# Kernel optimization log

Hardware: AMD Instinct MI355X
Metric: run time of the kernel (lower is better)

Reference implementation:

```python
import jax, jax.numpy as jnp
import numpy as np

V = 32000      # vocab_size
CTX = 1024     # context_length
D = 768        # n_embd
H = 12         # n_heads
HD = D // H    # head_dim
L = 6          # n_layers
DFF = 4 * D
B, S = 2, 1024
EPS = 1e-5


def _layernorm(x, w, b):
    mu = jnp.mean(x, axis=-1, keepdims=True)
    var = jnp.mean(jnp.square(x - mu), axis=-1, keepdims=True)
    return (x - mu) * jax.lax.rsqrt(var + EPS) * w + b


def setup_inputs() -> dict:
    key = jax.random.key(0)
    ks = iter(jax.random.split(key, 32))
    s = 0.02
    idx = jax.random.randint(next(ks), (B, S), 0, V)
    p = {
        "idx": idx,
        "tok_emb": jax.random.normal(next(ks), (V, D), jnp.float32) * s,
        "pos_emb": jax.random.normal(next(ks), (CTX, D), jnp.float32) * s,
        "ln1_w": jnp.ones((L, D)), "ln1_b": jnp.zeros((L, D)),
        "Wq": jax.random.normal(next(ks), (L, D, D), jnp.float32) * s,
        "bq": jnp.zeros((L, D)),
        "Wk": jax.random.normal(next(ks), (L, D, D), jnp.float32) * s,
        "bk": jnp.zeros((L, D)),
        "Wv": jax.random.normal(next(ks), (L, D, D), jnp.float32) * s,
        "bv": jnp.zeros((L, D)),
        "Wo": jax.random.normal(next(ks), (L, D, D), jnp.float32) * s,
        "bo": jnp.zeros((L, D)),
        "ln2_w": jnp.ones((L, D)), "ln2_b": jnp.zeros((L, D)),
        "W1": jax.random.normal(next(ks), (L, D, DFF), jnp.float32) * s,
        "b1": jnp.zeros((L, DFF)),
        "W2": jax.random.normal(next(ks), (L, DFF, D), jnp.float32) * s,
        "b2": jnp.zeros((L, D)),
        "lnf_w": jnp.ones((D,)), "lnf_b": jnp.zeros((D,)),
        "lm_head_w": jax.random.normal(next(ks), (D, V), jnp.float32) * s,
    }
    return p


def _forward(idx, tok_emb, pos_emb, ln1_w, ln1_b, Wq, bq, Wk, bk, Wv, bv,
             Wo, bo, ln2_w, ln2_b, W1, b1, W2, b2, lnf_w, lnf_b, lm_head_w):
    b, s = idx.shape
    x = tok_emb[idx] + pos_emb[:s]  # [B,S,D]
    mask = jnp.tril(jnp.ones((s, s), dtype=bool))  # causal
    scale = 1.0 / np.sqrt(HD)
    for l in range(L):
        # --- attention ---
        h = _layernorm(x, ln1_w[l], ln1_b[l])
        q = (h @ Wq[l] + bq[l]).reshape(b, s, H, HD).transpose(0, 2, 1, 3)
        k = (h @ Wk[l] + bk[l]).reshape(b, s, H, HD).transpose(0, 2, 1, 3)
        v = (h @ Wv[l] + bv[l]).reshape(b, s, H, HD).transpose(0, 2, 1, 3)
        att = jnp.einsum('bhqd,bhkd->bhqk', q, k) * scale
        att = jnp.where(mask, att, -jnp.inf)
        att = jax.nn.softmax(att, axis=-1)
        y = jnp.einsum('bhqk,bhkd->bhqd', att, v)
        y = y.transpose(0, 2, 1, 3).reshape(b, s, D)
        x = x + y @ Wo[l] + bo[l]
        # --- MLP ---
        h2 = _layernorm(x, ln2_w[l], ln2_b[l])
        x = x + jax.nn.relu(h2 @ W1[l] + b1[l]) @ W2[l] + b2[l]
    logits = _layernorm(x, lnf_w, lnf_b) @ lm_head_w  # [B,S,V]
    return logits


def reference(idx, tok_emb, pos_emb, ln1_w, ln1_b, Wq, bq, Wk, bk, Wv, bv,
              Wo, bo, ln2_w, ln2_b, W1, b1, W2, b2, lnf_w, lnf_b, lm_head_w):
    return _forward(idx, tok_emb, pos_emb, ln1_w, ln1_b, Wq, bq, Wk, bk, Wv,
                    bv, Wo, bo, ln2_w, ln2_b, W1, b1, W2, b2, lnf_w, lnf_b,
                    lm_head_w)
```

## Files before the change

### kernel.cpp

```cpp
#include <hip/hip_runtime.h>
#include <hip/hip_bf16.h>
#include <math.h>

#define D 768
#define NH 12
#define HD 64
#define NL 6
#define DFF 3072
#define BB 2
#define SS 1024
#define NROWS (BB*SS)
#define VOCAB 32000
#define QKVN (3*D)
#define LN_EPS 1e-5f

typedef __attribute__((ext_vector_type(8))) short bf16x8;
typedef __attribute__((ext_vector_type(4))) float f32x4;

typedef __attribute__((address_space(1))) const unsigned char* gas_ptr;
typedef __attribute__((address_space(3))) unsigned char* las_ptr;

__device__ __forceinline__ void load_lds16(const void* g, void* l) {
    __builtin_amdgcn_global_load_lds((gas_ptr)g, (las_ptr)l, 16, 0, 0);
}

__device__ __forceinline__ void storeOut(float* p, float v) { *p = v; }
__device__ __forceinline__ void storeOut(__hip_bfloat16* p, float v) { *p = __float2bfloat16(v); }
__device__ __forceinline__ ushort f2bs(float f) {
    __hip_bfloat16 h = __float2bfloat16(f);
    return *(ushort*)&h;
}

#define WAIT_VMCNT(n) asm volatile("s_waitcnt vmcnt(" #n ")" ::: "memory")

__global__ void embed_kernel(const int* __restrict__ idx, const float* __restrict__ tok,
                             const float* __restrict__ pos, float* __restrict__ x) {
    int row = blockIdx.x;
    int s = row % SS;
    int t = idx[row];
    for (int c = threadIdx.x; c < D; c += blockDim.x)
        x[row*D + c] = tok[(size_t)t*D + c] + pos[s*D + c];
}

template<typename OT>
__global__ __launch_bounds__(256) void layernorm_kernel(const float* __restrict__ x,
                                                        const float* __restrict__ w,
                                                        const float* __restrict__ b,
                                                        OT* __restrict__ out) {
    int row = blockIdx.x;
    __shared__ float l1[4], l2[4];
    int base = row * D;
    float vals[3];
    float s1 = 0.f, s2 = 0.f;
#pragma unroll
    for (int i = 0; i < 3; i++) {
        float v = x[base + threadIdx.x + i*256];
        vals[i] = v; s1 += v; s2 += v*v;
    }
#pragma unroll
    for (int o = 32; o > 0; o >>= 1) {
        s1 += __shfl_down(s1, o, 64);
        s2 += __shfl_down(s2, o, 64);
    }
    if ((threadIdx.x & 63) == 0) { l1[threadIdx.x >> 6] = s1; l2[threadIdx.x >> 6] = s2; }
    __syncthreads();
    float sum   = l1[0] + l1[1] + l1[2] + l1[3];
    float sumsq = l2[0] + l2[1] + l2[2] + l2[3];
    float mu  = sum * (1.f / D);
    float var = sumsq * (1.f / D) - mu * mu;
    float inv = rsqrtf(var + LN_EPS);
#pragma unroll
    for (int i = 0; i < 3; i++) {
        int c = threadIdx.x + i*256;
        storeOut(&out[base + c], (vals[i] - mu) * inv * w[c] + b[c]);
    }
}

__global__ __launch_bounds__(256) void transpose_cvt(const float* __restrict__ src,
                                                     __hip_bfloat16* __restrict__ dst,
                                                     int K, int N,
                                                     size_t srcLayerStride, size_t dstLayerStride,
                                                     int dstRowOff) {
    int l = blockIdx.z;
    src += (size_t)l * srcLayerStride;
    dst += (size_t)l * dstLayerStride + (size_t)dstRowOff * K;
    __shared__ float t[32][33];
    int k0 = blockIdx.x*32, n0 = blockIdx.y*32;
    int tx = threadIdx.x & 31, ty = threadIdx.x >> 5;
    for (int i = ty; i < 32; i += 8) t[i][tx] = src[(size_t)(k0+i)*N + n0+tx];
    __syncthreads();
    for (int i = ty; i < 32; i += 8) dst[(size_t)(n0+i)*K + k0+tx] = __float2bfloat16(t[tx][i]);
}

__global__ __launch_bounds__(256) void qkvo_trans(const float* __restrict__ Wq,
                                                  const float* __restrict__ Wk,
                                                  const float* __restrict__ Wv,
                                                  const float* __restrict__ Wo,
                                                  __hip_bfloat16* __restrict__ qkvT,
                                                  __hip_bfloat16* __restrict__ WoT) {
    int z = blockIdx.z, l = z >> 2, m = z & 3;
    const float* src = (m==0 ? Wq : m==1 ? Wk : m==2 ? Wv : Wo) + (size_t)l*D*D;
    __hip_bfloat16* dst = (m < 3) ? qkvT + (size_t)l*QKVN*D + (size_t)m*D*D
                                  : WoT  + (size_t)l*D*D;
    __shared__ float t[32][33];
    int k0 = blockIdx.x*32, n0 = blockIdx.y*32;
    int tx = threadIdx.x & 31, ty = threadIdx.x >> 5;
    for (int i = ty; i < 32; i += 8) t[i][tx] = src[(size_t)(k0+i)*D + n0+tx];
    __syncthreads();
    for (int i = ty; i < 32; i += 8) dst[(size_t)(n0+i)*D + k0+tx] = __float2bfloat16(t[tx][i]);
}

__global__ void pack_qkv_bias(const float* __restrict__ bq, const float* __restrict__ bk,
                              const float* __restrict__ bv, float* __restrict__ dst) {
    int l = blockIdx.y;
    int i = blockIdx.x*256 + threadIdx.x;
    dst[l*QKVN + i]         = bq[l*D + i];
    dst[l*QKVN + D + i]     = bk[l*D + i];
    dst[l*QKVN + 2*D + i]   = bv[l*D + i];
}

#define GSTAGE(buf, k0) do {                                                     \
    _Pragma("unroll")                                                            \
    for (int i_ = 0; i_ < BM/64; i_++) {                                         \
        int rt_ = wid*(BM/4) + i_*16;                                            \
        load_lds16(A + (size_t)(bm + rt_ + lrow)*K + (k0) + lcol,                \
                   &As[buf][rt_][0]);                                            \
    }                                                                            \
    _Pragma("unroll")                                                            \
    for (int i_ = 0; i_ < BN/64; i_++) {                                         \
        int rt_ = wid*(BN/4) + i_*16;                                            \
        load_lds16(BT + (size_t)(bn + rt_ + lrow)*K + (k0) + lcol,               \
                   &Bs[buf][rt_][0]);                                            \
    } } while (0)

template<int BM, int BN, int CMAJ, typename OT, int RELU, int RESID, int HASB, int VSTORE>
__global__ __launch_bounds__(256) void gemm_mfma(const ushort* __restrict__ A,
                                                 const ushort* __restrict__ BT,
                                                 const float* __restrict__ bias,
                                                 const float* __restrict__ X,
                                                 OT* __restrict__ C,
                                                 ushort* __restrict__ vt,
                                                 int N, int K, int gx, int gy) {
    constexpr int WTM = BM/2, WTN = BN/2;
    constexpr int FRM = BM/32, FRN = BN/32;
    __shared__ ushort As[2][BM][32];
    __shared__ ushort Bs[2][BN][32];

    int id = blockIdx.x;
    int swz = (id & 7) * (gridDim.x >> 3) + (id >> 3);
    int bx, by;
    if (CMAJ) { bx = swz / gy; by = swz - bx * gy; }
    else      { by = swz / gx; bx = swz - by * gx; }
    int bm = by * BM, bn = bx * BN;

    int tid = threadIdx.x;
    int lane = tid & 63, wid = tid >> 6;
    int wr = wid >> 1, wc = wid & 1;
    int lrow = lane >> 2;
    int lcol = (((lane & 3) ^ ((lane >> 3) & 3)) * 8);
    int fr = lane & 15, fc = lane >> 4;
    int rchunk = (fc ^ ((fr >> 1) & 3)) * 8;

    f32x4 acc[FRM][FRN];
#pragma unroll
    for (int i = 0; i < FRM; i++)
#pragma unroll
        for (int j = 0; j < FRN; j++)
#pragma unroll
            for (int r = 0; r < 4; r++) acc[i][j][r] = 0.f;

    GSTAGE(0, 0);
    asm volatile("s_waitcnt vmcnt(0)" ::: "memory");
    __syncthreads();

    int cur = 0;
    for (int t = 0; t < K/32; t++) {
        if (t*32 + 32 < K) GSTAGE(cur^1, t*32 + 32);
        bf16x8 af[FRM], bf[FRN];
#pragma unroll
        for (int mi = 0; mi < FRM; mi++)
            af[mi] = *(const bf16x8*)&As[cur][wr*WTM + mi*16 + fr][rchunk];
#pragma unroll
        for (int ni = 0; ni < FRN; ni++)
            bf[ni] = *(const bf16x8*)&Bs[cur][wc*WTN + ni*16 + fr][rchunk];
        __builtin_amdgcn_s_setprio(1);
#pragma unroll
        for (int mi = 0; mi < FRM; mi++)
#pragma unroll
            for (int ni = 0; ni < FRN; ni++)
                acc[mi][ni] = __builtin_amdgcn_mfma_f32_16x16x32_bf16(af[mi], bf[ni], acc[mi][ni], 0, 0, 0);
        __builtin_amdgcn_s_setprio(0);
        asm volatile("s_waitcnt vmcnt(0)" ::: "memory");
        __syncthreads();
        cur ^= 1;
    }

    if (VSTORE && bn >= 2*D) {
        int hh = (bn - 2*D) / HD;
        int b  = bm >> 10;
        size_t vbase = ((size_t)(b*NH + hh)) * HD;
        int srow0 = (bm & (SS-1)) + wr*WTM + fc*4;
#pragma unroll
        for (int mi = 0; mi < FRM; mi++) {
#pragma unroll
            for (int ni = 0; ni < FRN; ni++) {
                int col = bn + wc*WTN + ni*16 + fr;
                int d   = wc*WTN + ni*16 + fr;
                float bv_ = bias[col];
                ushort4 u;
                u.x = f2bs(acc[mi][ni][0] + bv_);
                u.y = f2bs(acc[mi][ni][1] + bv_);
                u.z = f2bs(acc[mi][ni][2] + bv_);
                u.w = f2bs(acc[mi][ni][3] + bv_);
                *(ushort4*)&vt[(vbase + d)*SS + srow0 + mi*16] = u;
            }
        }
    } else {
#pragma unroll
        for (int mi = 0; mi < FRM; mi++) {
#pragma unroll
            for (int r = 0; r < 4; r++) {
                int row = bm + wr*WTM + mi*16 + fc*4 + r;
#pragma unroll
                for (int ni = 0; ni < FRN; ni++) {
                    int col = bn + wc*WTN + ni*16 + fr;
                    float v = acc[mi][ni][r];
                    if (HASB) v += bias[col];
                    if (RESID) v += X[(size_t)row * N + col];
                    if (RELU) v = fmaxf(v, 0.f);
                    storeOut(&C[(size_t)row * N + col], v);
                }
            }
        }
    }
}

#define RSTAGE(slot, k0) do {                                                    \
    int row_ = tid >> 2;                                                         \
    load_lds16(A  + (size_t)(bm + row_)*K + (k0) + sc_,                          \
               (char*)As + (size_t)(slot)*4096 + (size_t)wid*1024);              \
    load_lds16(BT + (size_t)(bn + row_)*K + (k0) + sc_,                          \
               (char*)Bs + (size_t)(slot)*4096 + (size_t)wid*1024);              \
    } while (0)

template<int RELU>
__global__ __launch_bounds__(256) void gemm_ring64(const ushort* __restrict__ A,
                                                   const ushort* __restrict__ BT,
                                                   const float* __restrict__ bias,
                                                   const float* __restrict__ X,
                                                   float* __restrict__ C,
                                                   int N, int K, int gx) {
    __shared__ ushort As[4][64][32];
    __shared__ ushort Bs[4][64][32];

    int id = blockIdx.x;
    int swz = (id & 7) * (gridDim.x >> 3) + (id >> 3);
    int by = swz / gx, bx = swz - by * gx;
    int bm = by * 64, bn = bx * 64;

    int tid = threadIdx.x;
    int lane = tid & 63, wid = tid >> 6;
    int wr = wid >> 1, wc = wid & 1;
    int sc_ = ((lane & 3) ^ ((lane >> 3) & 3)) * 8;
    int fr = lane & 15, fc = lane >> 4;
    int rchunk = (fc ^ ((fr >> 1) & 3)) * 8;

    f32x4 acc[2][2];
#pragma unroll
    for (int i = 0; i < 2; i++)
#pragma unroll
        for (int j = 0; j < 2; j++)
#pragma unroll
            for (int r = 0; r < 4; r++) acc[i][j][r] = 0.f;

    const int NT = K / 32;
    RSTAGE(0, 0);
    RSTAGE(1, 32);
    RSTAGE(2, 64);

    for (int t = 0; t < NT; t++) {
        if (t < NT-2)      WAIT_VMCNT(4);
        else if (t == NT-2) WAIT_VMCNT(2);
        else               WAIT_VMCNT(0);
        __builtin_amdgcn_s_barrier();
        asm volatile("" ::: "memory");
        if (t + 3 < NT) RSTAGE((t+3) & 3, (t+3)*32);
        int s = t & 3;
        bf16x8 af[2], bf[2];
#pragma unroll
        for (int mi = 0; mi < 2; mi++)
            af[mi] = *(const bf16x8*)&As[s][wr*32 + mi*16 + fr][rchunk];
#pragma unroll
        for (int ni = 0; ni < 2; ni++)
            bf[ni] = *(const bf16x8*)&Bs[s][wc*32 + ni*16 + fr][rchunk];
        __builtin_amdgcn_s_setprio(1);
#pragma unroll
        for (int mi = 0; mi < 2; mi++)
#pragma unroll
            for (int ni = 0; ni < 2; ni++)
                acc[mi][ni] = __builtin_amdgcn_mfma_f32_16x16x32_bf16(af[mi], bf[ni], acc[mi][ni], 0, 0, 0);
        __builtin_amdgcn_s_setprio(0);
    }

#pragma unroll
    for (int mi = 0; mi < 2; mi++) {
#pragma unroll
        for (int r = 0; r < 4; r++) {
            int row = bm + wr*32 + mi*16 + fc*4 + r;
#pragma unroll
            for (int ni = 0; ni < 2; ni++) {
                int col = bn + wc*32 + ni*16 + fr;
                float v = acc[mi][ni][r] + bias[col] + X[(size_t)row * N + col];
                if (RELU) v = fmaxf(v, 0.f);
                C[(size_t)row * N + col] = v;
            }
        }
    }
}

#define LMSA3(slot, k0) do {                                                      \
    _Pragma("unroll")                                                             \
    for (int i_ = 0; i_ < 2; i_++) {                                              \
        int row_ = i_*128 + (tid >> 2);                                           \
        load_lds16(A + (size_t)(bm + row_)*D + (k0) + sc_,                        \
                   (char*)As3 + (size_t)(slot)*16384 + (size_t)(i_*512 + wid*64)*16); \
    } } while (0)
#define LMSB3(slot, k0) do {                                                      \
    _Pragma("unroll")                                                             \
    for (int i_ = 0; i_ < 2; i_++) {                                              \
        int row_ = i_*128 + (tid >> 2);                                           \
        load_lds16(BT + (size_t)(bm_n + row_)*D + (k0) + sc_,                     \
                   (char*)Bs3 + (size_t)(slot)*16384 + (size_t)(i_*512 + wid*64)*16); \
    } } while (0)

__global__ __launch_bounds__(512) void lm256_gemm(const ushort* __restrict__ A,
                                                  const ushort* __restrict__ BT,
                                                  float* __restrict__ C) {
    constexpr int NKT = D / 32;
    __shared__ ushort As3[3][256][32];
    __shared__ ushort Bs3[3][256][32];

    int id = blockIdx.x;
    int swz = (id & 7) * 125 + (id >> 3);
    int by = swz & 7;
    int bx = swz >> 3;
    int bm = by * 256, bm_n = bx * 256;

    int tid = threadIdx.x;
    int lane = tid & 63, wid = tid >> 6;
    int wr = wid >> 2, wc = wid & 3;
    int sc_ = ((tid & 3) ^ ((tid >> 3) & 3)) * 8;
    int fr = lane & 15, fc = lane >> 4;
    int rch = (fc ^ ((fr >> 1) & 3)) * 8;

    f32x4 acc[8][4];
#pragma unroll
    for (int i = 0; i < 8; i++)
#pragma unroll
        for (int j = 0; j < 4; j++)
#pragma unroll
            for (int r = 0; r < 4; r++) acc[i][j][r] = 0.f;

    LMSA3(0, 0);  LMSB3(0, 0);
    LMSA3(1, 32); LMSB3(1, 32);
    WAIT_VMCNT(4);
    __builtin_amdgcn_s_barrier();

    int s = 0;
    for (int j = 0; j < NKT; j++) {
        int s2 = s + 2; if (s2 >= 3) s2 -= 3;
        int kf2 = (j + 2) * 32;
        bf16x8 bfr[4], af[4];
#pragma unroll
        for (int ni = 0; ni < 4; ni++)
            bfr[ni] = *(const bf16x8*)&Bs3[s][wc*64 + ni*16 + fr][rch];
#pragma unroll
        for (int dm = 0; dm < 4; dm++)
            af[dm] = *(const bf16x8*)&As3[s][wr*128 + dm*16 + fr][rch];
        if (j + 2 < NKT) LMSA3(s2, kf2);
        __builtin_amdgcn_s_barrier();
        __builtin_amdgcn_s_setprio(1);
#pragma unroll
        for (int dm = 0; dm < 4; dm++)
#pragma unroll
            for (int ni = 0; ni < 4; ni++)
                acc[dm][ni] = __builtin_amdgcn_mfma_f32_16x16x32_bf16(af[dm], bfr[ni], acc[dm][ni], 0, 0, 0);
        __builtin_amdgcn_s_setprio(0);
        __builtin_amdgcn_s_barrier();
#pragma unroll
        for (int dm = 0; dm < 4; dm++)
            af[dm] = *(const bf16x8*)&As3[s][wr*128 + (4+dm)*16 + fr][rch];
        if (j + 2 < NKT) { LMSB3(s2, kf2); WAIT_VMCNT(2); }
        else             { WAIT_VMCNT(0); }
        __builtin_amdgcn_s_barrier();
        __builtin_amdgcn_s_setprio(1);
#pragma unroll
        for (int dm = 0; dm < 4; dm++)
#pragma unroll
            for (int ni = 0; ni < 4; ni++)
                acc[4+dm][ni] = __builtin_amdgcn_mfma_f32_16x16x32_bf16(af[dm], bfr[ni], acc[4+dm][ni], 0, 0, 0);
        __builtin_amdgcn_s_setprio(0);
        __builtin_amdgcn_s_barrier();
        s = s + 1; if (s >= 3) s = 0;
    }

#pragma unroll
    for (int mi = 0; mi < 8; mi++)
#pragma unroll
        for (int r = 0; r < 4; r++) {
            int row = bm + wr*128 + mi*16 + fc*4 + r;
            float* cp = C + (size_t)row * VOCAB + bm_n + wc*64 + fr;
#pragma unroll
            for (int ni = 0; ni < 4; ni++)
                cp[ni*16] = acc[mi][ni][r];
        }
}

#define KVSTAGE(buf, kv0) do {                                                   \
    _Pragma("unroll")                                                            \
    for (int j_ = 0; j_ < 2; j_++) {                                             \
        int r_ = w*16 + j_*8 + srow8;                                            \
        load_lds16(qkv + (size_t)(b*SS + (kv0) + r_)*QKVN + D + h*HD + schunk*8, \
                   &Ks[buf][w*16 + j_*8][0]);                                    \
        load_lds16(vt + ((size_t)(b*NH + h)*HD + r_)*SS + (kv0) + schunk*8,      \
                   &Vs[buf][w*16 + j_*8][0]);                                    \
    } } while (0)

__global__ __launch_bounds__(256) void attn_mfma(const ushort* __restrict__ qkv,
                                                 const ushort* __restrict__ vt,
                                                 __hip_bfloat16* __restrict__ y) {
    const int bx = blockIdx.x;
    const int qt = 15 - (bx & 15);
    const int h  = (bx >> 4) % NH;
    const int b  = bx / (16*NH);
    const int tid  = threadIdx.x;
    const int lane = tid & 63, w = tid >> 6;
    const int fr = lane & 15, fc = lane >> 4;

    __shared__ ushort Qs[64][64];
    __shared__ ushort Ks[2][64][64];
    __shared__ ushort Vs[2][64][64];
    __shared__ ushort Ps[4][16][72];

    const int q0 = qt * 64;
    const int srow8  = lane >> 3;
    const int schunk = (lane & 7) ^ srow8;

#pragma unroll
    for (int j = 0; j < 2; j++) {
        int r = w*16 + j*8 + srow8;
        load_lds16(qkv + (size_t)(b*SS + q0 + r)*QKVN + h*HD + schunk*8, &Qs[w*16 + j*8][0]);
    }
    KVSTAGE(0, 0);
    asm volatile("s_waitcnt vmcnt(0)" ::: "memory");
    __syncthreads();
    bf16x8 qf[2];
#pragma unroll
    for (int s = 0; s < 2; s++)
        qf[s] = *(const bf16x8*)&Qs[w*16 + fr][((s*4 + fc) ^ (fr & 7))*8];

    f32x4 oacc[4];
#pragma unroll
    for (int ni = 0; ni < 4; ni++)
#pragma unroll
        for (int r = 0; r < 4; r++) oacc[ni][r] = 0.f;
    float m[4] = {-INFINITY, -INFINITY, -INFINITY, -INFINITY};
    float l[4] = {0.f, 0.f, 0.f, 0.f};

    int cur = 0;
    for (int kt = 0; kt <= qt; kt++) {
        if (kt < qt) KVSTAGE(cur^1, (kt+1)*64);
        f32x4 sacc[4];
#pragma unroll
        for (int ni = 0; ni < 4; ni++)
#pragma unroll
            for (int r = 0; r < 4; r++) sacc[ni][r] = 0.f;
#pragma unroll
        for (int ni = 0; ni < 4; ni++)
#pragma unroll
            for (int s = 0; s < 2; s++) {
                bf16x8 kf = *(const bf16x8*)&Ks[cur][ni*16 + fr][((s*4 + fc) ^ (fr & 7))*8];
                sacc[ni] = __builtin_amdgcn_mfma_f32_16x16x32_bf16(qf[s], kf, sacc[ni], 0, 0, 0);
            }
        if (kt == qt) {
#pragma unroll
            for (int ni = 0; ni < 4; ni++)
#pragma unroll
                for (int r = 0; r < 4; r++) {
                    float v = sacc[ni][r] * 0.125f;
                    sacc[ni][r] = (ni*16 + fr > w*16 + fc*4 + r) ? -INFINITY : v;
                }
        } else {
#pragma unroll
            for (int ni = 0; ni < 4; ni++)
#pragma unroll
                for (int r = 0; r < 4; r++) sacc[ni][r] *= 0.125f;
        }
        float p[4][4];
#pragma unroll
        for (int r = 0; r < 4; r++) {
            float mx = fmaxf(fmaxf(sacc[0][r], sacc[1][r]), fmaxf(sacc[2][r], sacc[3][r]));
#pragma unroll
            for (int o = 1; o < 16; o <<= 1) mx = fmaxf(mx, __shfl_xor(mx, o, 64));
            float mn = fmaxf(m[r], mx);
            float fac = __expf(m[r] - mn);
            float rs = 0.f;
#pragma unroll
            for (int ni = 0; ni < 4; ni++) {
                float pv = __expf(sacc[ni][r] - mn);
                p[ni][r] = pv;
                rs += pv;
            }
#pragma unroll
            for (int o = 1; o < 16; o <<= 1) rs += __shfl_xor(rs, o, 64);
            l[r] = l[r] * fac + rs;
            m[r] = mn;
#pragma unroll
            for (int ni = 0; ni < 4; ni++) oacc[ni][r] *= fac;
        }
#pragma unroll
        for (int ni = 0; ni < 4; ni++)
#pragma unroll
            for (int r = 0; r < 4; r++)
                Ps[w][fc*4 + r][ni*16 + fr] = f2bs(p[ni][r]);
        bf16x8 pa[2];
#pragma unroll
        for (int s = 0; s < 2; s++) pa[s] = *(const bf16x8*)&Ps[w][fr][s*32 + fc*8];
#pragma unroll
        for (int ni = 0; ni < 4; ni++)
#pragma unroll
            for (int s = 0; s < 2; s++) {
                bf16x8 vf = *(const bf16x8*)&Vs[cur][ni*16 + fr][((s*4 + fc) ^ (fr & 7))*8];
                oacc[ni] = __builtin_amdgcn_mfma_f32_16x16x32_bf16(pa[s], vf, oacc[ni], 0, 0, 0);
            }
        asm volatile("s_waitcnt vmcnt(0)" ::: "memory");
        __syncthreads();
        cur ^= 1;
    }
#pragma unroll
    for (int r = 0; r < 4; r++) {
        float rinv = 1.f / l[r];
        int row = b*SS + q0 + w*16 + fc*4 + r;
#pragma unroll
        for (int ni = 0; ni < 4; ni++)
            y[(size_t)row*D + h*HD + ni*16 + fr] = __float2bfloat16(oacc[ni][r] * rinv);
    }
}

extern "C" void kernel_launch(void* const* d_in, const int* in_sizes, int n_in,
                              void* d_out, int out_size, void* d_ws, size_t ws_size,
                              hipStream_t stream) {
    const int*   idx  = (const int*)d_in[0];
    const float* tok  = (const float*)d_in[1];
    const float* pos  = (const float*)d_in[2];
    const float* ln1w = (const float*)d_in[3];
    const float* ln1b = (const float*)d_in[4];
    const float* Wq   = (const float*)d_in[5];
    const float* bq   = (const float*)d_in[6];
    const float* Wk   = (const float*)d_in[7];
    const float* bk   = (const float*)d_in[8];
    const float* Wv   = (const float*)d_in[9];
    const float* bv   = (const float*)d_in[10];
    const float* Wo   = (const float*)d_in[11];
    const float* bo   = (const float*)d_in[12];
    const float* ln2w = (const float*)d_in[13];
    const float* ln2b = (const float*)d_in[14];
    const float* W1   = (const float*)d_in[15];
    const float* b1   = (const float*)d_in[16];
    const float* W2   = (const float*)d_in[17];
    const float* b2   = (const float*)d_in[18];
    const float* lnfw = (const float*)d_in[19];
    const float* lnfb = (const float*)d_in[20];
    const float* lmw  = (const float*)d_in[21];
    float* out = (float*)d_out;

    char* p = (char*)d_ws;
    __hip_bfloat16* qkvT = (__hip_bfloat16*)p; p += (size_t)NL*QKVN*D*2;
    __hip_bfloat16* WoT  = (__hip_bfloat16*)p; p += (size_t)NL*D*D*2;
    __hip_bfloat16* W1T  = (__hip_bfloat16*)p; p += (size_t)NL*DFF*D*2;
    __hip_bfloat16* W2T  = (__hip_bfloat16*)p; p += (size_t)NL*D*DFF*2;
    __hip_bfloat16* lmT  = (__hip_bfloat16*)p; p += (size_t)VOCAB*D*2;
    float*          bqkv = (float*)p;          p += (size_t)NL*QKVN*4;
    float*          x    = (float*)p;          p += (size_t)NROWS*D*4;
    __hip_bfloat16* h    = (__hip_bfloat16*)p; p += (size_t)NROWS*D*2;
    __hip_bfloat16* qkv  = (__hip_bfloat16*)p; p += (size_t)NROWS*QKVN*2;
    __hip_bfloat16* vt   = (__hip_bfloat16*)p; p += (size_t)BB*NH*HD*SS*2;
    __hip_bfloat16* yb   = (__hip_bfloat16*)p; p += (size_t)NROWS*D*2;
    __hip_bfloat16* a1   = (__hip_bfloat16*)p; p += (size_t)NROWS*DFF*2;

    qkvo_trans<<<dim3(D/32, D/32, NL*4), 256, 0, stream>>>(Wq, Wk, Wv, Wo, qkvT, WoT);
    transpose_cvt<<<dim3(D/32, DFF/32, NL), 256, 0, stream>>>(W1, W1T, D, DFF, (size_t)D*DFF, (size_t)DFF*D, 0);
    transpose_cvt<<<dim3(DFF/32, D/32, NL), 256, 0, stream>>>(W2, W2T, DFF, D, (size_t)DFF*D, (size_t)D*DFF, 0);
    transpose_cvt<<<dim3(D/32, VOCAB/32, 1), 256, 0, stream>>>(lmw, lmT, D, VOCAB, 0, 0, 0);
    pack_qkv_bias<<<dim3(3, NL), 256, 0, stream>>>(bq, bk, bv, bqkv);

    embed_kernel<<<NROWS, 256, 0, stream>>>(idx, tok, pos, x);

    for (int l = 0; l < NL; l++) {
        layernorm_kernel<<<NROWS, 256, 0, stream>>>(x, ln1w + l*D, ln1b + l*D, h);
        gemm_mfma<128,64,0,__hip_bfloat16,0,0,1,1><<<576, 256, 0, stream>>>(
            (const ushort*)h, (const ushort*)(qkvT + (size_t)l*QKVN*D),
            bqkv + (size_t)l*QKVN, nullptr, qkv, (ushort*)vt, QKVN, D, QKVN/64, NROWS/128);
        attn_mfma<<<BB*NH*(SS/64), 256, 0, stream>>>((const ushort*)qkv, (const ushort*)vt, yb);
        gemm_ring64<0><<<384, 256, 0, stream>>>(
            (const ushort*)yb, (const ushort*)(WoT + (size_t)l*D*D),
            bo + (size_t)l*D, x, x, D, D, D/64);
        layernorm_kernel<<<NROWS, 256, 0, stream>>>(x, ln2w + l*D, ln2b + l*D, h);
        gemm_mfma<128,128,0,__hip_bfloat16,1,0,1,0><<<384, 256, 0, stream>>>(
            (const ushort*)h, (const ushort*)(W1T + (size_t)l*DFF*D),
            b1 + (size_t)l*DFF, nullptr, a1, nullptr, DFF, D, DFF/128, NROWS/128);
        gemm_ring64<0><<<384, 256, 0, stream>>>(
            (const ushort*)a1, (const ushort*)(W2T + (size_t)l*D*DFF),
            b2 + (size_t)l*D, x, x, D, DFF, D/64);
    }
    layernorm_kernel<<<NROWS, 256, 0, stream>>>(x, lnfw, lnfb, h);
    lm256_gemm<<<1000, 512, 0, stream>>>((const ushort*)h, (const ushort*)lmT, out);
}
```

Baseline: 1.195 ms.

## Deepen async LDS pipelines in GEMMs and attention with multi-stage rings

Replaces the double-buffered gemm_mfma with a 4-slot ring GEMM (128x64 tile) that issues loads three stages ahead and waits with partial vmcnt counts instead of a full drain. The FC1 GEMM moves from 128x128 to 128x64 tiles, giving more blocks. The residual ring GEMM deepens from 4 to 6 slots, and attention gets a 3-slot K/V ring with partial waits. The aim is to hide global-load latency behind MFMA work, at the cost of more LDS per block, which may lower occupancy.

```diff
diff --git a/kernel.cpp b/kernel.cpp
--- a/kernel.cpp
+++ b/kernel.cpp
@@ -119,93 +119,88 @@
     dst[l*QKVN + 2*D + i]   = bv[l*D + i];
 }
 
-#define GSTAGE(buf, k0) do {                                                     \
+#define RG_STAGE(slot, k0) do {                                                  \
     _Pragma("unroll")                                                            \
-    for (int i_ = 0; i_ < BM/64; i_++) {                                         \
-        int rt_ = wid*(BM/4) + i_*16;                                            \
-        load_lds16(A + (size_t)(bm + rt_ + lrow)*K + (k0) + lcol,                \
-                   &As[buf][rt_][0]);                                            \
-    }                                                                            \
-    _Pragma("unroll")                                                            \
-    for (int i_ = 0; i_ < BN/64; i_++) {                                         \
-        int rt_ = wid*(BN/4) + i_*16;                                            \
-        load_lds16(BT + (size_t)(bn + rt_ + lrow)*K + (k0) + lcol,               \
-                   &Bs[buf][rt_][0]);                                            \
-    } } while (0)
-
-template<int BM, int BN, int CMAJ, typename OT, int RELU, int RESID, int HASB, int VSTORE>
-__global__ __launch_bounds__(256) void gemm_mfma(const ushort* __restrict__ A,
-                                                 const ushort* __restrict__ BT,
-                                                 const float* __restrict__ bias,
-                                                 const float* __restrict__ X,
-                                                 OT* __restrict__ C,
-                                                 ushort* __restrict__ vt,
-                                                 int N, int K, int gx, int gy) {
-    constexpr int WTM = BM/2, WTN = BN/2;
-    constexpr int FRM = BM/32, FRN = BN/32;
-    __shared__ ushort As[2][BM][32];
-    __shared__ ushort Bs[2][BN][32];
+    for (int i_ = 0; i_ < 2; i_++)                                               \
+        load_lds16(A + (size_t)(bm + i_*64 + srow)*K + (k0) + sc_,               \
+                   &AsR[slot][i_*64 + wid*16][0]);                               \
+    load_lds16(BT + (size_t)(bn + srow)*K + (k0) + sc_,                          \
+               &BsR[slot][wid*16][0]);                                           \
+    } while (0)
+
+template<typename OT, int RELU, int HASB, int VSTORE>
+__global__ __launch_bounds__(256) void rg_gemm(const ushort* __restrict__ A,
+                                               const ushort* __restrict__ BT,
+                                               const float* __restrict__ bias,
+                                               OT* __restrict__ C,
+                                               ushort* __restrict__ vt,
+                                               int N, int K, int gx) {
+    constexpr int BM = 128, BN = 64;
+    __shared__ ushort AsR[4][BM][32];
+    __shared__ ushort BsR[4][BN][32];
 
     int id = blockIdx.x;
     int swz = (id & 7) * (gridDim.x >> 3) + (id >> 3);
-    int bx, by;
-    if (CMAJ) { bx = swz / gy; by = swz - bx * gy; }
-    else      { by = swz / gx; bx = swz - by * gx; }
+    int by = swz / gx, bx = swz - by * gx;
     int bm = by * BM, bn = bx * BN;
 
     int tid = threadIdx.x;
     int lane = tid & 63, wid = tid >> 6;
     int wr = wid >> 1, wc = wid & 1;
-    int lrow = lane >> 2;
-    int lcol = (((lane & 3) ^ ((lane >> 3) & 3)) * 8);
+    int srow = tid >> 2;
+    int sc_ = ((tid & 3) ^ ((tid >> 3) & 3)) * 8;
     int fr = lane & 15, fc = lane >> 4;
     int rchunk = (fc ^ ((fr >> 1) & 3)) * 8;
 
-    f32x4 acc[FRM][FRN];
-#pragma unroll
-    for (int i = 0; i < FRM; i++)
-#pragma unroll
-        for (int j = 0; j < FRN; j++)
+    f32x4 acc[4][2];
+#pragma unroll
+    for (int i = 0; i < 4; i++)
+#pragma unroll
+        for (int j = 0; j < 2; j++)
 #pragma unroll
             for (int r = 0; r < 4; r++) acc[i][j][r] = 0.f;
 
-    GSTAGE(0, 0);
-    asm volatile("s_waitcnt vmcnt(0)" ::: "memory");
-    __syncthreads();
-
-    int cur = 0;
-    for (int t = 0; t < K/32; t++) {
-        if (t*32 + 32 < K) GSTAGE(cur^1, t*32 + 32);
-        bf16x8 af[FRM], bf[FRN];
-#pragma unroll
-        for (int mi = 0; mi < FRM; mi++)
-            af[mi] = *(const bf16x8*)&As[cur][wr*WTM + mi*16 + fr][rchunk];
-#pragma unroll
-        for (int ni = 0; ni < FRN; ni++)
-            bf[ni] = *(const bf16x8*)&Bs[cur][wc*WTN + ni*16 + fr][rchunk];
+    const int NT = K / 32;
+    RG_STAGE(0, 0);
+    RG_STAGE(1, 32);
+    RG_STAGE(2, 64);
+
+    for (int t = 0; t < NT; t++) {
+        int rem = NT - 1 - t;
+        if (rem >= 2)      WAIT_VMCNT(6);
+        else if (rem == 1) WAIT_VMCNT(3);
+        else               WAIT_VMCNT(0);
+        __builtin_amdgcn_s_barrier();
+        asm volatile("" ::: "memory");
+        if (t + 3 < NT) RG_STAGE((t+3) & 3, (t+3)*32);
+        int s = t & 3;
+        bf16x8 af[4], bf[2];
+#pragma unroll
+        for (int mi = 0; mi < 4; mi++)
+            af[mi] = *(const bf16x8*)&AsR[s][wr*64 + mi*16 + fr][rchunk];
+#pragma unroll
+        for (int ni = 0; ni < 2; ni++)
+            bf[ni] = *(const bf16x8*)&BsR[s][wc*32 + ni*16 + fr][rchunk];
         __builtin_amdgcn_s_setprio(1);
 #pragma unroll
-        for (int mi = 0; mi < FRM; mi++)
-#pragma unroll
-            for (int ni = 0; ni < FRN; ni++)
+        for (int mi = 0; mi < 4; mi++)
+#pragma unroll
+            for (int ni = 0; ni < 2; ni++)
                 acc[mi][ni] = __builtin_amdgcn_mfma_f32_16x16x32_bf16(af[mi], bf[ni], acc[mi][ni], 0, 0, 0);
         __builtin_amdgcn_s_setprio(0);
-        asm volatile("s_waitcnt vmcnt(0)" ::: "memory");
-        __syncthreads();
-        cur ^= 1;
     }
 
     if (VSTORE && bn >= 2*D) {
         int hh = (bn - 2*D) / HD;
         int b  = bm >> 10;
         size_t vbase = ((size_t)(b*NH + hh)) * HD;
-        int srow0 = (bm & (SS-1)) + wr*WTM + fc*4;
-#pragma unroll
-        for (int mi = 0; mi < FRM; mi++) {
-#pragma unroll
-            for (int ni = 0; ni < FRN; ni++) {
-                int col = bn + wc*WTN + ni*16 + fr;
-                int d   = wc*WTN + ni*16 + fr;
+        int srow0 = (bm & (SS-1)) + wr*64 + fc*4;
+#pragma unroll
+        for (int mi = 0; mi < 4; mi++) {
+#pragma unroll
+            for (int ni = 0; ni < 2; ni++) {
+                int col = bn + wc*32 + ni*16 + fr;
+                int d   = wc*32 + ni*16 + fr;
                 float bv_ = bias[col];
                 ushort4 u;
                 u.x = f2bs(acc[mi][ni][0] + bv_);
@@ -217,16 +212,15 @@
         }
     } else {
 #pragma unroll
-        for (int mi = 0; mi < FRM; mi++) {
+        for (int mi = 0; mi < 4; mi++) {
 #pragma unroll
             for (int r = 0; r < 4; r++) {
-                int row = bm + wr*WTM + mi*16 + fc*4 + r;
-#pragma unroll
-                for (int ni = 0; ni < FRN; ni++) {
-                    int col = bn + wc*WTN + ni*16 + fr;
+                int row = bm + wr*64 + mi*16 + fc*4 + r;
+#pragma unroll
+                for (int ni = 0; ni < 2; ni++) {
+                    int col = bn + wc*32 + ni*16 + fr;
                     float v = acc[mi][ni][r];
                     if (HASB) v += bias[col];
-                    if (RESID) v += X[(size_t)row * N + col];
                     if (RELU) v = fmaxf(v, 0.f);
                     storeOut(&C[(size_t)row * N + col], v);
                 }
@@ -250,8 +244,8 @@
                                                    const float* __restrict__ X,
                                                    float* __restrict__ C,
                                                    int N, int K, int gx) {
-    __shared__ ushort As[4][64][32];
-    __shared__ ushort Bs[4][64][32];
+    __shared__ ushort As[6][64][32];
+    __shared__ ushort Bs[6][64][32];
 
     int id = blockIdx.x;
     int swz = (id & 7) * (gridDim.x >> 3) + (id >> 3);
@@ -277,15 +271,20 @@
     RSTAGE(0, 0);
     RSTAGE(1, 32);
     RSTAGE(2, 64);
+    RSTAGE(3, 96);
+    RSTAGE(4, 128);
 
     for (int t = 0; t < NT; t++) {
-        if (t < NT-2)      WAIT_VMCNT(4);
-        else if (t == NT-2) WAIT_VMCNT(2);
+        int rem = NT - t;
+        if (rem >= 5)      WAIT_VMCNT(8);
+        else if (rem == 4) WAIT_VMCNT(6);
+        else if (rem == 3) WAIT_VMCNT(4);
+        else if (rem == 2) WAIT_VMCNT(2);
         else               WAIT_VMCNT(0);
         __builtin_amdgcn_s_barrier();
         asm volatile("" ::: "memory");
-        if (t + 3 < NT) RSTAGE((t+3) & 3, (t+3)*32);
-        int s = t & 3;
+        if (t + 5 < NT) RSTAGE((t+5) % 6, (t+5)*32);
+        int s = t % 6;
         bf16x8 af[2], bf[2];
 #pragma unroll
         for (int mi = 0; mi < 2; mi++)
@@ -438,8 +437,8 @@
     const int fr = lane & 15, fc = lane >> 4;
 
     __shared__ ushort Qs[64][64];
-    __shared__ ushort Ks[2][64][64];
-    __shared__ ushort Vs[2][64][64];
+    __shared__ ushort Ks[3][64][64];
+    __shared__ ushort Vs[3][64][64];
     __shared__ ushort Ps[4][16][72];
 
     const int q0 = qt * 64;
@@ -452,12 +451,12 @@
         load_lds16(qkv + (size_t)(b*SS + q0 + r)*QKVN + h*HD + schunk*8, &Qs[w*16 + j*8][0]);
     }
     KVSTAGE(0, 0);
-    asm volatile("s_waitcnt vmcnt(0)" ::: "memory");
-    __syncthreads();
+    if (qt >= 1) { KVSTAGE(1, 64); WAIT_VMCNT(4); }
+    else         { WAIT_VMCNT(0); }
     bf16x8 qf[2];
 #pragma unroll
-    for (int s = 0; s < 2; s++)
-        qf[s] = *(const bf16x8*)&Qs[w*16 + fr][((s*4 + fc) ^ (fr & 7))*8];
+    for (int s_ = 0; s_ < 2; s_++)
+        qf[s_] = *(const bf16x8*)&Qs[w*16 + fr][((s_*4 + fc) ^ (fr & 7))*8];
 
     f32x4 oacc[4];
 #pragma unroll
@@ -467,9 +466,16 @@
     float m[4] = {-INFINITY, -INFINITY, -INFINITY, -INFINITY};
     float l[4] = {0.f, 0.f, 0.f, 0.f};
 
-    int cur = 0;
+    int s = 0;
     for (int kt = 0; kt <= qt; kt++) {
-        if (kt < qt) KVSTAGE(cur^1, (kt+1)*64);
+        if (kt < qt) WAIT_VMCNT(4);
+        else         WAIT_VMCNT(0);
+        __builtin_amdgcn_s_barrier();
+        asm volatile("" ::: "memory");
+        if (kt + 2 <= qt) {
+            int s2 = s + 2; if (s2 >= 3) s2 -= 3;
+            KVSTAGE(s2, (kt+2)*64);
+        }
         f32x4 sacc[4];
 #pragma unroll
         for (int ni = 0; ni < 4; ni++)
@@ -478,9 +484,9 @@
 #pragma unroll
         for (int ni = 0; ni < 4; ni++)
 #pragma unroll
-            for (int s = 0; s < 2; s++) {
-                bf16x8 kf = *(const bf16x8*)&Ks[cur][ni*16 + fr][((s*4 + fc) ^ (fr & 7))*8];
-                sacc[ni] = __builtin_amdgcn_mfma_f32_16x16x32_bf16(qf[s], kf, sacc[ni], 0, 0, 0);
+            for (int s_ = 0; s_ < 2; s_++) {
+                bf16x8 kf = *(const bf16x8*)&Ks[s][ni*16 + fr][((s_*4 + fc) ^ (fr & 7))*8];
+                sacc[ni] = __builtin_amdgcn_mfma_f32_16x16x32_bf16(qf[s_], kf, sacc[ni], 0, 0, 0);
             }
         if (kt == qt) {
 #pragma unroll
@@ -525,17 +531,15 @@
                 Ps[w][fc*4 + r][ni*16 + fr] = f2bs(p[ni][r]);
         bf16x8 pa[2];
 #pragma unroll
-        for (int s = 0; s < 2; s++) pa[s] = *(const bf16x8*)&Ps[w][fr][s*32 + fc*8];
+        for (int s_ = 0; s_ < 2; s_++) pa[s_] = *(const bf16x8*)&Ps[w][fr][s_*32 + fc*8];
 #pragma unroll
         for (int ni = 0; ni < 4; ni++)
 #pragma unroll
-            for (int s = 0; s < 2; s++) {
-                bf16x8 vf = *(const bf16x8*)&Vs[cur][ni*16 + fr][((s*4 + fc) ^ (fr & 7))*8];
-                oacc[ni] = __builtin_amdgcn_mfma_f32_16x16x32_bf16(pa[s], vf, oacc[ni], 0, 0, 0);
+            for (int s_ = 0; s_ < 2; s_++) {
+                bf16x8 vf = *(const bf16x8*)&Vs[s][ni*16 + fr][((s_*4 + fc) ^ (fr & 7))*8];
+                oacc[ni] = __builtin_amdgcn_mfma_f32_16x16x32_bf16(pa[s_], vf, oacc[ni], 0, 0, 0);
             }
-        asm volatile("s_waitcnt vmcnt(0)" ::: "memory");
-        __syncthreads();
-        cur ^= 1;
+        s = s + 1; if (s >= 3) s = 0;
     }
 #pragma unroll
     for (int r = 0; r < 4; r++) {
@@ -598,17 +602,17 @@
 
     for (int l = 0; l < NL; l++) {
         layernorm_kernel<<<NROWS, 256, 0, stream>>>(x, ln1w + l*D, ln1b + l*D, h);
-        gemm_mfma<128,64,0,__hip_bfloat16,0,0,1,1><<<576, 256, 0, stream>>>(
+        rg_gemm<__hip_bfloat16,0,1,1><<<576, 256, 0, stream>>>(
             (const ushort*)h, (const ushort*)(qkvT + (size_t)l*QKVN*D),
-            bqkv + (size_t)l*QKVN, nullptr, qkv, (ushort*)vt, QKVN, D, QKVN/64, NROWS/128);
+            bqkv + (size_t)l*QKVN, qkv, (ushort*)vt, QKVN, D, QKVN/64);
         attn_mfma<<<BB*NH*(SS/64), 256, 0, stream>>>((const ushort*)qkv, (const ushort*)vt, yb);
         gemm_ring64<0><<<384, 256, 0, stream>>>(
             (const ushort*)yb, (const ushort*)(WoT + (size_t)l*D*D),
             bo + (size_t)l*D, x, x, D, D, D/64);
         layernorm_kernel<<<NROWS, 256, 0, stream>>>(x, ln2w + l*D, ln2b + l*D, h);
-        gemm_mfma<128,128,0,__hip_bfloat16,1,0,1,0><<<384, 256, 0, stream>>>(
+        rg_gemm<__hip_bfloat16,1,1,0><<<768, 256, 0, stream>>>(
             (const ushort*)h, (const ushort*)(W1T + (size_t)l*DFF*D),
-            b1 + (size_t)l*DFF, nullptr, a1, nullptr, DFF, D, DFF/128, NROWS/128);
+            b1 + (size_t)l*DFF, a1, nullptr, DFF, D, DFF/64);
         gemm_ring64<0><<<384, 256, 0, stream>>>(
             (const ushort*)a1, (const ushort*)(W2T + (size_t)l*D*DFF),
             b2 + (size_t)l*D, x, x, D, DFF, D/64);
```

After: 1.191 ms, median of 2. No clear change (-0.3%).
